# Kernel optimization log

Hardware: AMD Instinct MI355X
Metric: run time of the kernel (lower is better)

The kernel has to match this reference:

```python
import jax, jax.numpy as jnp
import numpy as np

N = 100000        # nodes
E = 1600000       # directed edges (avg degree 16)
F_IN, F_HID, F_OUT = 512, 32, 16


def setup_inputs() -> dict:
    key = jax.random.key(0)
    k0, k1, k2, k3 = jax.random.split(key, 4)
    x = jax.random.normal(k0, (N, F_IN), dtype=jnp.float32)
    edge_index = jax.random.randint(k1, (2, E), 0, N, dtype=jnp.int32)
    # Glorot-ish init for the two GCNConv linear weights
    W1 = jax.random.normal(k2, (F_IN, F_HID), dtype=jnp.float32) / np.float32(np.sqrt(F_IN))
    W2 = jax.random.normal(k3, (F_HID, F_OUT), dtype=jnp.float32) / np.float32(np.sqrt(F_HID))
    b1 = jnp.zeros((F_HID,), jnp.float32)
    b2 = jnp.zeros((F_OUT,), jnp.float32)
    return {"x": x, "W1": W1, "b1": b1, "W2": W2, "b2": b2, "edge_index": edge_index}


def gcn_conv(x, W, b, src, dst):
    """PyG GCNConv: h = x W; symmetric-normalized aggregation with self-loops; + bias."""
    h = x @ W                                   # [N, F_out] project first (PyG order)
    # degree including the implicit self-loop (start from ones)
    deg = jnp.ones((N,), h.dtype).at[dst].add(1.0)
    dinv = jax.lax.rsqrt(deg)                   # deg^{-1/2}
    coef = (dinv[src] * dinv[dst])[:, None]     # [E, 1] edge norm
    msg = h[src] * coef                         # gather + scale
    agg = jax.ops.segment_sum(msg, dst, num_segments=N)  # scatter-add to dst
    agg = agg + h * (dinv * dinv)[:, None]      # self-loop contribution
    return agg + b


def reference(x, W1, b1, W2, b2, edge_index):
    src, dst = edge_index[0], edge_index[1]
    h = jax.nn.relu(gcn_conv(x, W1, b1, src, dst))
    # F.dropout(training=self.training) is identity in eval mode
    h = gcn_conv(h, W2, b2, src, dst)
    return jax.nn.log_softmax(h, axis=1)
```

## Files before the change

### kernel.cpp

```cpp
#include <hip/hip_runtime.h>
#include <hip/hip_bf16.h>
#include <cstdint>

#define NN   100000
#define NE   1600000
#define FIN  512
#define FHID 32
#define FOUT 16

#define BSHIFT 8
#define BSIZE  256
#define NBUCK  391
#define HB     128
#define BEPB   4096
#define NBB    ((NE + BEPB - 1) / BEPB)
#define GB     782

typedef float f32x4 __attribute__((ext_vector_type(4)));
typedef short s16x8 __attribute__((ext_vector_type(8)));
typedef short s16x4 __attribute__((ext_vector_type(4)));
typedef int   i32x4 __attribute__((ext_vector_type(4)));
typedef unsigned int u32;
typedef unsigned short u16;

__device__ __forceinline__ short f2bf(float f) {
  union { float f; uint32_t u; } v; v.f = f;
  uint32_t r = v.u + 0x7fffu + ((v.u >> 16) & 1u);
  return (short)(r >> 16);
}
__device__ __forceinline__ float bf2f(u16 u) {
  union { uint32_t u; float f; } v; v.u = (uint32_t)u << 16; return v.f;
}

__global__ __launch_bounds__(256) void k_hist(const int* __restrict__ dst,
                                              u32* __restrict__ bcount) {
  __shared__ u32 h[NBUCK];
  int tid = threadIdx.x;
  for (int i = tid; i < NBUCK; i += 256) h[i] = 0;
  __syncthreads();
  const int stride = HB * 256 * 4;
  for (int e0 = (blockIdx.x * 256 + tid) * 4; e0 + 3 < NE; e0 += stride) {
    i32x4 d4 = *(const i32x4*)(dst + e0);
    atomicAdd(&h[d4[0] >> BSHIFT], 1u);
    atomicAdd(&h[d4[1] >> BSHIFT], 1u);
    atomicAdd(&h[d4[2] >> BSHIFT], 1u);
    atomicAdd(&h[d4[3] >> BSHIFT], 1u);
  }
  __syncthreads();
  for (int i = tid; i < NBUCK; i += 256)
    if (h[i]) atomicAdd(&bcount[i], h[i]);
}

__global__ __launch_bounds__(512) void k_bscan(const u32* __restrict__ bc,
                                               u32* __restrict__ bstart,
                                               u32* __restrict__ bcur,
                                               const float* __restrict__ W1,
                                               u16* __restrict__ wfrag) {
  __shared__ u32 tmp[512];
  int tid = threadIdx.x;
  u32 v = (tid < NBUCK) ? bc[tid] : 0;
  tmp[tid] = v;
  __syncthreads();
  #pragma unroll
  for (int off = 1; off < 512; off <<= 1) {
    u32 t = (tid >= off) ? tmp[tid - off] : 0;
    __syncthreads();
    tmp[tid] += t;
    __syncthreads();
  }
  if (tid < NBUCK) { u32 e = tmp[tid] - v; bstart[tid] = e; bcur[tid] = e; }
  if (tid == 511) bstart[NBUCK] = tmp[511];

  for (int it = 0; it < 32; ++it) {
    int flat = it * 512 + tid;
    int i  = flat & 7;
    int l  = (flat >> 3) & 63;
    int nt = (flat >> 9) & 1;
    int kt = flat >> 10;
    int k  = kt * 32 + ((l >> 4) << 3) + i;
    int n  = nt * 16 + (l & 15);
    wfrag[flat] = (u16)f2bf(W1[k * 32 + n]);
  }
}

__global__ __launch_bounds__(512) void k_bin(const int* __restrict__ src,
                                             const int* __restrict__ dst,
                                             u32* __restrict__ bcur,
                                             u32* __restrict__ binned) {
  __shared__ u32 cnt[NBUCK];
  __shared__ u32 lofs[NBUCK];
  __shared__ u32 gbase[NBUCK];
  __shared__ u32 tmp[512];
  __shared__ u32 stage[BEPB];
  __shared__ u16 sb[BEPB];
  int tid = threadIdx.x;
  for (int i = tid; i < NBUCK; i += 512) cnt[i] = 0;
  __syncthreads();

  int base = blockIdx.x * BEPB;
  u32 vals[8]; u32 ofs[8]; int bks[8];
  #pragma unroll
  for (int half = 0; half < 2; ++half) {
    int e0 = base + tid * 8 + half * 4;
    if (e0 + 3 < NE) {
      i32x4 s4 = *(const i32x4*)(src + e0);
      i32x4 d4 = *(const i32x4*)(dst + e0);
      #pragma unroll
      for (int k = 0; k < 4; ++k) {
        int b = d4[k] >> BSHIFT;
        bks[half * 4 + k] = b;
        vals[half * 4 + k] = (u32)s4[k] | ((u32)(d4[k] & (BSIZE - 1)) << 17);
        ofs[half * 4 + k] = atomicAdd(&cnt[b], 1u);
      }
    } else {
      #pragma unroll
      for (int k = 0; k < 4; ++k) {
        int e = e0 + k;
        bool ok = e < NE;
        int s = 0, d = 0;
        if (ok) { s = src[e]; d = dst[e]; }
        int b = ok ? (d >> BSHIFT) : -1;
        bks[half * 4 + k] = b;
        vals[half * 4 + k] = (u32)s | ((u32)(d & (BSIZE - 1)) << 17);
        ofs[half * 4 + k] = ok ? atomicAdd(&cnt[b], 1u) : 0;
      }
    }
  }
  __syncthreads();

  u32 cv = (tid < NBUCK) ? cnt[tid] : 0;
  tmp[tid] = cv;
  __syncthreads();
  #pragma unroll
  for (int off = 1; off < 512; off <<= 1) {
    u32 t = (tid >= off) ? tmp[tid - off] : 0;
    __syncthreads();
    tmp[tid] += t;
    __syncthreads();
  }
  if (tid < NBUCK) {
    lofs[tid] = tmp[tid] - cv;
    gbase[tid] = cv ? atomicAdd(&bcur[tid], cv) : 0;
  }
  __syncthreads();
  u32 total = tmp[511];
  __syncthreads();

  #pragma unroll
  for (int k = 0; k < 8; ++k) {
    if (bks[k] >= 0) {
      u32 sl = lofs[bks[k]] + ofs[k];
      stage[sl] = vals[k];
      sb[sl] = (u16)bks[k];
    }
  }
  __syncthreads();

  for (u32 s2 = tid; s2 < total; s2 += 512) {
    int b = sb[s2];
    binned[gbase[b] + (s2 - lofs[b])] = stage[s2];
  }
}

__global__ __launch_bounds__(256) void k_fin(const u32* __restrict__ binned,
                                             const u32* __restrict__ bstart,
                                             int* __restrict__ deg,
                                             int* __restrict__ rs,
                                             float* __restrict__ dinv,
                                             int* __restrict__ csr) {
  __shared__ u32 degl[BSIZE];
  __shared__ u32 rsl[BSIZE];
  int tid = threadIdx.x;
  int b = blockIdx.x;
  u32 start = bstart[b];
  u32 n = bstart[b + 1] - start;

  degl[tid] = 0;
  __syncthreads();
  for (u32 k = tid; k < n; k += 256)
    atomicAdd(&degl[binned[start + k] >> 17], 1u);
  __syncthreads();

  u32 v = degl[tid];
  rsl[tid] = v;
  __syncthreads();
  #pragma unroll
  for (int off = 1; off < 256; off <<= 1) {
    u32 t = (tid >= off) ? rsl[tid - off] : 0;
    __syncthreads();
    rsl[tid] += t;
    __syncthreads();
  }
  u32 e = rsl[tid] - v;
  __syncthreads();
  rsl[tid] = e;

  int g = b * BSIZE + tid;
  if (g < NN) {
    deg[g] = (int)v;
    rs[g] = (int)(start + e);
    dinv[g] = rsqrtf(1.0f + (float)v);
  }
  __syncthreads();

  for (u32 k = tid; k < n; k += 256) {
    u32 vv = binned[start + k];
    u32 pos = atomicAdd(&rsl[vv >> 17], 1u);
    csr[start + pos] = (int)(vv & 0x1FFFFu);
  }
}

#define G1_ISSUE(TILE)                                                        \
  do {                                                                        \
    int r0_ = (TILE) * 16;                                                    \
    _Pragma("unroll")                                                         \
    for (int r_ = 0; r_ < 16; ++r_) {                                         \
      int row_ = r0_ + r_;                                                    \
      if (row_ >= NN) row_ = NN - 1;                                          \
      const float* rp_ = x + (size_t)row_ * FIN + lane * 4;                   \
      va[r_] = *(const f32x4*)rp_;                                            \
      vb[r_] = *(const f32x4*)(rp_ + 256);                                    \
    }                                                                         \
  } while (0)

#define G1_CVTWRITE()                                                         \
  do {                                                                        \
    _Pragma("unroll")                                                         \
    for (int r_ = 0; r_ < 16; ++r_) {                                         \
      u32 sw_ = (u32)((r_ & 7) << 4);                                         \
      s16x4 w0_, w1_;                                                         \
      _Pragma("unroll")                                                       \
      for (int q_ = 0; q_ < 4; ++q_) {                                        \
        w0_[q_] = f2bf(va[r_][q_]);                                           \
        w1_[q_] = f2bf(vb[r_][q_]);                                           \
      }                                                                       \
      *(s16x4*)(xw + (((u32)(r_ * 1024 + lane * 8)) ^ sw_)) = w0_;            \
      *(s16x4*)(xw + (((u32)(r_ * 1024 + 512 + lane * 8)) ^ sw_)) = w1_;      \
    }                                                                         \
  } while (0)

#define G1_MFMA_STORE(TILE)                                                   \
  do {                                                                        \
    f32x4 acc0_ = {}, acc1_ = {};                                             \
    _Pragma("unroll")                                                         \
    for (int kt_ = 0; kt_ < 16; ++kt_) {                                      \
      s16x8 af_ = *(const s16x8*)(xw +                                        \
          (((u32)(m * 1024 + kt_ * 64 + h * 16)) ^ msw));                     \
      s16x8 b0_ = wf[(kt_ * 2 + 0) * 64 + lane];                              \
      s16x8 b1_ = wf[(kt_ * 2 + 1) * 64 + lane];                              \
      acc0_ = __builtin_amdgcn_mfma_f32_16x16x32_bf16(af_, b0_, acc0_, 0,0,0);\
      acc1_ = __builtin_amdgcn_mfma_f32_16x16x32_bf16(af_, b1_, acc1_, 0,0,0);\
    }                                                                         \
    int r0_ = (TILE) * 16;                                                    \
    _Pragma("unroll")                                                         \
    for (int r_ = 0; r_ < 4; ++r_) {                                          \
      int row_ = r0_ + h * 4 + r_;                                            \
      if (row_ < NN) {                                                        \
        float di_ = dinv[row_];                                               \
        u16* o_ = Hs1 + (size_t)row_ * FHID + m;                              \
        o_[0]  = (u16)f2bf(acc0_[r_] * di_);                                  \
        o_[16] = (u16)f2bf(acc1_[r_] * di_);                                  \
      }                                                                       \
    }                                                                         \
  } while (0)

__global__ __launch_bounds__(256) void k_gemm1(const float* __restrict__ x,
                                               const u16* __restrict__ wfrag,
                                               const float* __restrict__ dinv,
                                               u16* __restrict__ Hs1) {
  __shared__ u16 Xs[4][16][512];
  const int tid  = threadIdx.x;
  const int lane = tid & 63;
  const int wv   = tid >> 6;
  char* xw = (char*)&Xs[wv][0][0];
  const int h = lane >> 4;
  const int m = lane & 15;
  const u32 msw = (u32)((m & 7) << 4);
  const s16x8* wf = (const s16x8*)wfrag;

  const int t0 = (blockIdx.x * 4 + wv) * 2;
  f32x4 va[16], vb[16];

  G1_ISSUE(t0);
  G1_CVTWRITE();
  G1_ISSUE(t0 + 1);
  G1_MFMA_STORE(t0);
  G1_CVTWRITE();
  G1_MFMA_STORE(t0 + 1);
}

__global__ __launch_bounds__(256) void k_gat1(const int* __restrict__ csr,
                                              const int* __restrict__ rs,
                                              const int* __restrict__ deg,
                                              const float* __restrict__ dinv,
                                              const float* __restrict__ b1,
                                              const float* __restrict__ W2,
                                              const u16* __restrict__ Hs1,
                                              u16* __restrict__ Hs2) {
  __shared__ float w[FHID * FOUT];
  for (int i = threadIdx.x; i < FHID * FOUT; i += 256) w[i] = W2[i];
  __syncthreads();

  int t = blockIdx.x * 256 + threadIdx.x;
  int d = t >> 2;
  if (d >= NN) return;
  int p = t & 3;
  int start = rs[d], n = deg[d];

  float a0[8], a1[8], a2[8], a3[8];
  {
    s16x8 v = *(const s16x8*)(Hs1 + (size_t)d * FHID + p * 8);
    #pragma unroll
    for (int k = 0; k < 8; ++k) {
      a0[k] = bf2f((u16)v[k]); a1[k] = 0.f; a2[k] = 0.f; a3[k] = 0.f;
    }
  }
  int j = 0;
  for (; j + 8 <= n; j += 8) {
    int s0=csr[start+j],   s1=csr[start+j+1], s2=csr[start+j+2], s3=csr[start+j+3];
    int s4=csr[start+j+4], s5=csr[start+j+5], s6=csr[start+j+6], s7=csr[start+j+7];
    s16x8 v0 = *(const s16x8*)(Hs1 + (size_t)s0 * FHID + p * 8);
    s16x8 v1 = *(const s16x8*)(Hs1 + (size_t)s1 * FHID + p * 8);
    s16x8 v2 = *(const s16x8*)(Hs1 + (size_t)s2 * FHID + p * 8);
    s16x8 v3 = *(const s16x8*)(Hs1 + (size_t)s3 * FHID + p * 8);
    s16x8 v4 = *(const s16x8*)(Hs1 + (size_t)s4 * FHID + p * 8);
    s16x8 v5 = *(const s16x8*)(Hs1 + (size_t)s5 * FHID + p * 8);
    s16x8 v6 = *(const s16x8*)(Hs1 + (size_t)s6 * FHID + p * 8);
    s16x8 v7 = *(const s16x8*)(Hs1 + (size_t)s7 * FHID + p * 8);
    #pragma unroll
    for (int k = 0; k < 8; ++k) {
      a0[k] += bf2f((u16)v0[k]);
      a1[k] += bf2f((u16)v1[k]);
      a2[k] += bf2f((u16)v2[k]);
      a3[k] += bf2f((u16)v3[k]);
      a0[k] += bf2f((u16)v4[k]);
      a1[k] += bf2f((u16)v5[k]);
      a2[k] += bf2f((u16)v6[k]);
      a3[k] += bf2f((u16)v7[k]);
    }
  }
  for (; j + 4 <= n; j += 4) {
    int s0=csr[start+j], s1=csr[start+j+1], s2=csr[start+j+2], s3=csr[start+j+3];
    s16x8 v0 = *(const s16x8*)(Hs1 + (size_t)s0 * FHID + p * 8);
    s16x8 v1 = *(const s16x8*)(Hs1 + (size_t)s1 * FHID + p * 8);
    s16x8 v2 = *(const s16x8*)(Hs1 + (size_t)s2 * FHID + p * 8);
    s16x8 v3 = *(const s16x8*)(Hs1 + (size_t)s3 * FHID + p * 8);
    #pragma unroll
    for (int k = 0; k < 8; ++k) {
      a0[k] += bf2f((u16)v0[k]);
      a1[k] += bf2f((u16)v1[k]);
      a2[k] += bf2f((u16)v2[k]);
      a3[k] += bf2f((u16)v3[k]);
    }
  }
  for (; j < n; ++j) {
    int s0 = csr[start + j];
    s16x8 v0 = *(const s16x8*)(Hs1 + (size_t)s0 * FHID + p * 8);
    #pragma unroll
    for (int k = 0; k < 8; ++k) a0[k] += bf2f((u16)v0[k]);
  }

  float dd = dinv[d];
  float h[8];
  #pragma unroll
  for (int k = 0; k < 8; ++k)
    h[k] = fmaxf(((a0[k] + a1[k]) + (a2[k] + a3[k])) * dd + b1[p * 8 + k], 0.0f);

  float pj[FOUT];
  #pragma unroll
  for (int jj = 0; jj < FOUT; ++jj) pj[jj] = 0.f;
  #pragma unroll
  for (int k = 0; k < 8; ++k)
    #pragma unroll
    for (int jj = 0; jj < FOUT; ++jj)
      pj[jj] = fmaf(h[k], w[(p * 8 + k) * FOUT + jj], pj[jj]);
  #pragma unroll
  for (int jj = 0; jj < FOUT; ++jj) {
    pj[jj] += __shfl_xor(pj[jj], 1);
    pj[jj] += __shfl_xor(pj[jj], 2);
  }
  s16x4 o;
  #pragma unroll
  for (int q = 0; q < 4; ++q) o[q] = f2bf(pj[p * 4 + q] * dd);
  *(s16x4*)(Hs2 + (size_t)d * FOUT + p * 4) = o;
}

__global__ __launch_bounds__(256) void k_gat2(const int* __restrict__ csr,
                                              const int* __restrict__ rs,
                                              const int* __restrict__ deg,
                                              const float* __restrict__ dinv,
                                              const float* __restrict__ b2,
                                              const u16* __restrict__ Hs2,
                                              float* __restrict__ out) {
  int t = blockIdx.x * 256 + threadIdx.x;
  int d = t >> 2;
  if (d >= NN) return;
  int p = t & 3;
  int start = rs[d], n = deg[d];

  float a0[4], a1[4], a2[4], a3[4];
  {
    s16x4 v = *(const s16x4*)(Hs2 + (size_t)d * FOUT + p * 4);
    #pragma unroll
    for (int k = 0; k < 4; ++k) { a0[k] = bf2f((u16)v[k]); a1[k]=0.f; a2[k]=0.f; a3[k]=0.f; }
  }
  int j = 0;
  for (; j + 8 <= n; j += 8) {
    int s0=csr[start+j],   s1=csr[start+j+1], s2=csr[start+j+2], s3=csr[start+j+3];
    int s4=csr[start+j+4], s5=csr[start+j+5], s6=csr[start+j+6], s7=csr[start+j+7];
    s16x4 v0 = *(const s16x4*)(Hs2 + (size_t)s0 * FOUT + p * 4);
    s16x4 v1 = *(const s16x4*)(Hs2 + (size_t)s1 * FOUT + p * 4);
    s16x4 v2 = *(const s16x4*)(Hs2 + (size_t)s2 * FOUT + p * 4);
    s16x4 v3 = *(const s16x4*)(Hs2 + (size_t)s3 * FOUT + p * 4);
    s16x4 v4 = *(const s16x4*)(Hs2 + (size_t)s4 * FOUT + p * 4);
    s16x4 v5 = *(const s16x4*)(Hs2 + (size_t)s5 * FOUT + p * 4);
    s16x4 v6 = *(const s16x4*)(Hs2 + (size_t)s6 * FOUT + p * 4);
    s16x4 v7 = *(const s16x4*)(Hs2 + (size_t)s7 * FOUT + p * 4);
    #pragma unroll
    for (int k = 0; k < 4; ++k) {
      a0[k] += bf2f((u16)v0[k]); a1[k] += bf2f((u16)v1[k]);
      a2[k] += bf2f((u16)v2[k]); a3[k] += bf2f((u16)v3[k]);
      a0[k] += bf2f((u16)v4[k]); a1[k] += bf2f((u16)v5[k]);
      a2[k] += bf2f((u16)v6[k]); a3[k] += bf2f((u16)v7[k]);
    }
  }
  for (; j + 4 <= n; j += 4) {
    int s0=csr[start+j], s1=csr[start+j+1], s2=csr[start+j+2], s3=csr[start+j+3];
    s16x4 v0 = *(const s16x4*)(Hs2 + (size_t)s0 * FOUT + p * 4);
    s16x4 v1 = *(const s16x4*)(Hs2 + (size_t)s1 * FOUT + p * 4);
    s16x4 v2 = *(const s16x4*)(Hs2 + (size_t)s2 * FOUT + p * 4);
    s16x4 v3 = *(const s16x4*)(Hs2 + (size_t)s3 * FOUT + p * 4);
    #pragma unroll
    for (int k = 0; k < 4; ++k) {
      a0[k] += bf2f((u16)v0[k]); a1[k] += bf2f((u16)v1[k]);
      a2[k] += bf2f((u16)v2[k]); a3[k] += bf2f((u16)v3[k]);
    }
  }
  for (; j < n; ++j) {
    int s0 = csr[start + j];
    s16x4 v0 = *(const s16x4*)(Hs2 + (size_t)s0 * FOUT + p * 4);
    #pragma unroll
    for (int k = 0; k < 4; ++k) a0[k] += bf2f((u16)v0[k]);
  }

  float dd = dinv[d];
  float z[4];
  #pragma unroll
  for (int k = 0; k < 4; ++k)
    z[k] = ((a0[k]+a1[k]) + (a2[k]+a3[k])) * dd + b2[p * 4 + k];

  float m = fmaxf(fmaxf(z[0], z[1]), fmaxf(z[2], z[3]));
  m = fmaxf(m, __shfl_xor(m, 1));
  m = fmaxf(m, __shfl_xor(m, 2));
  float s = expf(z[0]-m) + expf(z[1]-m) + expf(z[2]-m) + expf(z[3]-m);
  s += __shfl_xor(s, 1);
  s += __shfl_xor(s, 2);
  float lse = m + logf(s);

  f32x4 o = { z[0]-lse, z[1]-lse, z[2]-lse, z[3]-lse };
  *(f32x4*)(out + (size_t)d * FOUT + p * 4) = o;
}

extern "C" void kernel_launch(void* const* d_in, const int* in_sizes, int n_in,
                              void* d_out, int out_size, void* d_ws, size_t ws_size,
                              hipStream_t stream) {
  const float* x  = (const float*)d_in[0];
  const float* W1 = (const float*)d_in[1];
  const float* b1 = (const float*)d_in[2];
  const float* W2 = (const float*)d_in[3];
  const float* b2 = (const float*)d_in[4];
  const int*   ei = (const int*)d_in[5];
  const int* srcv = ei;
  const int* dstv = ei + NE;

  char* ws = (char*)d_ws;
  const size_t KB = 1024, MB = 1048576;
  u32*   bcount = (u32*)(ws + 0);
  u32*   bstart = (u32*)(ws + 8 * KB);
  u32*   bcur   = (u32*)(ws + 16 * KB);
  u16*   wfrag  = (u16*)(ws + 64 * KB);
  int*   deg    = (int*)(ws + 512 * KB);
  int*   rs     = (int*)(ws + 1024 * KB);
  float* dinv   = (float*)(ws + 1536 * KB);
  u32*   binned = (u32*)(ws + 2 * MB);
  int*   csr    = (int*)(ws + 9 * MB);
  u16*   Hs1    = (u16*)(ws + 16 * MB);
  u16*   Hs2    = (u16*)(ws + 23 * MB);
  float* out    = (float*)d_out;

  hipMemsetAsync(bcount, 0, NBUCK * sizeof(u32), stream);

  k_hist <<<HB,  256, 0, stream>>>(dstv, bcount);
  k_bscan<<<1,   512, 0, stream>>>(bcount, bstart, bcur, W1, wfrag);
  k_bin  <<<NBB, 512, 0, stream>>>(srcv, dstv, bcur, binned);
  k_fin  <<<NBUCK, 256, 0, stream>>>(binned, bstart, deg, rs, dinv, csr);
  k_gemm1<<<GB, 256, 0, stream>>>(x, wfrag, dinv, Hs1);
  k_gat1 <<<(NN * 4 + 255) / 256, 256, 0, stream>>>(csr, rs, deg, dinv, b1, W2, Hs1, Hs2);
  k_gat2 <<<(NN * 4 + 255) / 256, 256, 0, stream>>>(csr, rs, deg, dinv, b2, Hs2, out);
}
```

Before: 139.2 us.

## Fuse bucket scan into histogram and co-schedule GEMM with edge binning

Folds the single-block bucket scan and W1 fragment conversion into the histogram kernel, using a last-block ticket so the scan needs no separate launch. Merges the layer-1 GEMM and the edge binning into one heterogeneous launch, which requires removing the GEMM's dependency on dinv: H1 is stored unscaled and the source-side dinv is applied per edge in the first gather. This removes two launches and lets the GEMM's memory traffic overlap with binning. In exchange the first gather does an extra random dinv load per edge, and the bin block size is halved to fit 256-thread blocks.

```diff
diff --git a/kernel.cpp b/kernel.cpp
--- a/kernel.cpp
+++ b/kernel.cpp
@@ -12,9 +12,10 @@
 #define BSIZE  256
 #define NBUCK  391
 #define HB     128
-#define BEPB   4096
+#define BEPB   2048
 #define NBB    ((NE + BEPB - 1) / BEPB)
-#define GB     782
+#define GEMB   391
+#define TOTB   (GEMB + NBB)
 
 typedef float f32x4 __attribute__((ext_vector_type(4)));
 typedef short s16x8 __attribute__((ext_vector_type(8)));
@@ -33,9 +34,31 @@
 }
 
 __global__ __launch_bounds__(256) void k_hist(const int* __restrict__ dst,
-                                              u32* __restrict__ bcount) {
+                                              const float* __restrict__ W1,
+                                              u16* __restrict__ wfrag,
+                                              u32* __restrict__ bcount,
+                                              u32* __restrict__ ticket,
+                                              u32* __restrict__ bstart,
+                                              u32* __restrict__ bcur) {
   __shared__ u32 h[NBUCK];
+  __shared__ u32 wsum[4];
+  __shared__ bool amlast;
   int tid = threadIdx.x;
+  int lane = tid & 63;
+
+  if (blockIdx.x == 0) {
+    for (int it = 0; it < 64; ++it) {
+      int flat = it * 256 + tid;
+      int i  = flat & 7;
+      int l  = (flat >> 3) & 63;
+      int nt = (flat >> 9) & 1;
+      int kt = flat >> 10;
+      int k  = kt * 32 + ((l >> 4) << 3) + i;
+      int n  = nt * 16 + (l & 15);
+      wfrag[flat] = (u16)f2bf(W1[k * 32 + n]);
+    }
+  }
+
   for (int i = tid; i < NBUCK; i += 256) h[i] = 0;
   __syncthreads();
   const int stride = HB * 256 * 4;
@@ -49,166 +72,50 @@
   __syncthreads();
   for (int i = tid; i < NBUCK; i += 256)
     if (h[i]) atomicAdd(&bcount[i], h[i]);
-}
-
-__global__ __launch_bounds__(512) void k_bscan(const u32* __restrict__ bc,
-                                               u32* __restrict__ bstart,
-                                               u32* __restrict__ bcur,
-                                               const float* __restrict__ W1,
-                                               u16* __restrict__ wfrag) {
-  __shared__ u32 tmp[512];
-  int tid = threadIdx.x;
-  u32 v = (tid < NBUCK) ? bc[tid] : 0;
-  tmp[tid] = v;
-  __syncthreads();
-  #pragma unroll
-  for (int off = 1; off < 512; off <<= 1) {
-    u32 t = (tid >= off) ? tmp[tid - off] : 0;
-    __syncthreads();
-    tmp[tid] += t;
-    __syncthreads();
-  }
-  if (tid < NBUCK) { u32 e = tmp[tid] - v; bstart[tid] = e; bcur[tid] = e; }
-  if (tid == 511) bstart[NBUCK] = tmp[511];
-
-  for (int it = 0; it < 32; ++it) {
-    int flat = it * 512 + tid;
-    int i  = flat & 7;
-    int l  = (flat >> 3) & 63;
-    int nt = (flat >> 9) & 1;
-    int kt = flat >> 10;
-    int k  = kt * 32 + ((l >> 4) << 3) + i;
-    int n  = nt * 16 + (l & 15);
-    wfrag[flat] = (u16)f2bf(W1[k * 32 + n]);
-  }
-}
-
-__global__ __launch_bounds__(512) void k_bin(const int* __restrict__ src,
-                                             const int* __restrict__ dst,
-                                             u32* __restrict__ bcur,
-                                             u32* __restrict__ binned) {
-  __shared__ u32 cnt[NBUCK];
-  __shared__ u32 lofs[NBUCK];
-  __shared__ u32 gbase[NBUCK];
-  __shared__ u32 tmp[512];
-  __shared__ u32 stage[BEPB];
-  __shared__ u16 sb[BEPB];
-  int tid = threadIdx.x;
-  for (int i = tid; i < NBUCK; i += 512) cnt[i] = 0;
-  __syncthreads();
-
-  int base = blockIdx.x * BEPB;
-  u32 vals[8]; u32 ofs[8]; int bks[8];
-  #pragma unroll
-  for (int half = 0; half < 2; ++half) {
-    int e0 = base + tid * 8 + half * 4;
-    if (e0 + 3 < NE) {
-      i32x4 s4 = *(const i32x4*)(src + e0);
-      i32x4 d4 = *(const i32x4*)(dst + e0);
-      #pragma unroll
-      for (int k = 0; k < 4; ++k) {
-        int b = d4[k] >> BSHIFT;
-        bks[half * 4 + k] = b;
-        vals[half * 4 + k] = (u32)s4[k] | ((u32)(d4[k] & (BSIZE - 1)) << 17);
-        ofs[half * 4 + k] = atomicAdd(&cnt[b], 1u);
-      }
-    } else {
-      #pragma unroll
-      for (int k = 0; k < 4; ++k) {
-        int e = e0 + k;
-        bool ok = e < NE;
-        int s = 0, d = 0;
-        if (ok) { s = src[e]; d = dst[e]; }
-        int b = ok ? (d >> BSHIFT) : -1;
-        bks[half * 4 + k] = b;
-        vals[half * 4 + k] = (u32)s | ((u32)(d & (BSIZE - 1)) << 17);
-        ofs[half * 4 + k] = ok ? atomicAdd(&cnt[b], 1u) : 0;
-      }
-    }
-  }
-  __syncthreads();
-
-  u32 cv = (tid < NBUCK) ? cnt[tid] : 0;
-  tmp[tid] = cv;
-  __syncthreads();
-  #pragma unroll
-  for (int off = 1; off < 512; off <<= 1) {
-    u32 t = (tid >= off) ? tmp[tid - off] : 0;
-    __syncthreads();
-    tmp[tid] += t;
-    __syncthreads();
-  }
-  if (tid < NBUCK) {
-    lofs[tid] = tmp[tid] - cv;
-    gbase[tid] = cv ? atomicAdd(&bcur[tid], cv) : 0;
-  }
-  __syncthreads();
-  u32 total = tmp[511];
-  __syncthreads();
-
-  #pragma unroll
-  for (int k = 0; k < 8; ++k) {
-    if (bks[k] >= 0) {
-      u32 sl = lofs[bks[k]] + ofs[k];
-      stage[sl] = vals[k];
-      sb[sl] = (u16)bks[k];
-    }
-  }
-  __syncthreads();
-
-  for (u32 s2 = tid; s2 < total; s2 += 512) {
-    int b = sb[s2];
-    binned[gbase[b] + (s2 - lofs[b])] = stage[s2];
-  }
-}
-
-__global__ __launch_bounds__(256) void k_fin(const u32* __restrict__ binned,
-                                             const u32* __restrict__ bstart,
-                                             int* __restrict__ deg,
-                                             int* __restrict__ rs,
-                                             float* __restrict__ dinv,
-                                             int* __restrict__ csr) {
-  __shared__ u32 degl[BSIZE];
-  __shared__ u32 rsl[BSIZE];
-  int tid = threadIdx.x;
-  int b = blockIdx.x;
-  u32 start = bstart[b];
-  u32 n = bstart[b + 1] - start;
-
-  degl[tid] = 0;
-  __syncthreads();
-  for (u32 k = tid; k < n; k += 256)
-    atomicAdd(&degl[binned[start + k] >> 17], 1u);
-  __syncthreads();
-
-  u32 v = degl[tid];
-  rsl[tid] = v;
-  __syncthreads();
-  #pragma unroll
-  for (int off = 1; off < 256; off <<= 1) {
-    u32 t = (tid >= off) ? rsl[tid - off] : 0;
-    __syncthreads();
-    rsl[tid] += t;
-    __syncthreads();
-  }
-  u32 e = rsl[tid] - v;
-  __syncthreads();
-  rsl[tid] = e;
-
-  int g = b * BSIZE + tid;
-  if (g < NN) {
-    deg[g] = (int)v;
-    rs[g] = (int)(start + e);
-    dinv[g] = rsqrtf(1.0f + (float)v);
-  }
-  __syncthreads();
-
-  for (u32 k = tid; k < n; k += 256) {
-    u32 vv = binned[start + k];
-    u32 pos = atomicAdd(&rsl[vv >> 17], 1u);
-    csr[start + pos] = (int)(vv & 0x1FFFFu);
-  }
-}
+  __syncthreads();
+  if (tid == 0) {
+    __threadfence();
+    u32 t = __hip_atomic_fetch_add(ticket, 1u, __ATOMIC_ACQ_REL, __HIP_MEMORY_SCOPE_AGENT);
+    amlast = (t == gridDim.x - 1);
+  }
+  __syncthreads();
+  if (!amlast) return;
+
+  u32 a0 = (2*tid   < NBUCK) ? __hip_atomic_load(&bcount[2*tid],   __ATOMIC_RELAXED, __HIP_MEMORY_SCOPE_AGENT) : 0;
+  u32 a1 = (2*tid+1 < NBUCK) ? __hip_atomic_load(&bcount[2*tid+1], __ATOMIC_RELAXED, __HIP_MEMORY_SCOPE_AGENT) : 0;
+  u32 s = a0 + a1;
+  u32 v = s;
+  #pragma unroll
+  for (int off = 1; off < 64; off <<= 1) {
+    u32 t = __shfl_up(v, off);
+    if (lane >= off) v += t;
+  }
+  if (lane == 63) wsum[tid >> 6] = v;
+  __syncthreads();
+  if (tid < 4) {
+    u32 w0 = wsum[tid], w = w0;
+    #pragma unroll
+    for (int off = 1; off < 4; off <<= 1) {
+      u32 t = __shfl_up(w, off, 4);
+      if ((tid & 3) >= off) w += t;
+    }
+    wsum[tid] = w - w0;
+  }
+  __syncthreads();
+  u32 excl = v - s + wsum[tid >> 6];
+  if (2*tid < NBUCK)   { bstart[2*tid]   = excl;      bcur[2*tid]   = excl; }
+  if (2*tid+1 < NBUCK) { bstart[2*tid+1] = excl + a0; bcur[2*tid+1] = excl + a0; }
+  if (tid == 255) bstart[NBUCK] = excl + s;
+}
+
+union BGSh {
+  u16 Xs[4][16][512];
+  struct {
+    u32 cnt[NBUCK]; u32 lofs[NBUCK]; u32 gbase[NBUCK];
+    u32 wsum[4]; u32 total;
+    u32 stage[BEPB]; u16 sb[BEPB];
+  } bin;
+};
 
 #define G1_ISSUE(TILE)                                                        \
   do {                                                                        \
@@ -256,37 +163,175 @@
     for (int r_ = 0; r_ < 4; ++r_) {                                          \
       int row_ = r0_ + h * 4 + r_;                                            \
       if (row_ < NN) {                                                        \
-        float di_ = dinv[row_];                                               \
-        u16* o_ = Hs1 + (size_t)row_ * FHID + m;                              \
-        o_[0]  = (u16)f2bf(acc0_[r_] * di_);                                  \
-        o_[16] = (u16)f2bf(acc1_[r_] * di_);                                  \
+        u16* o_ = H1 + (size_t)row_ * FHID + m;                               \
+        o_[0]  = (u16)f2bf(acc0_[r_]);                                        \
+        o_[16] = (u16)f2bf(acc1_[r_]);                                        \
       }                                                                       \
     }                                                                         \
   } while (0)
 
-__global__ __launch_bounds__(256) void k_gemm1(const float* __restrict__ x,
-                                               const u16* __restrict__ wfrag,
-                                               const float* __restrict__ dinv,
-                                               u16* __restrict__ Hs1) {
-  __shared__ u16 Xs[4][16][512];
-  const int tid  = threadIdx.x;
+__global__ __launch_bounds__(256) void k_binemm(
+    const int* __restrict__ src, const int* __restrict__ dst,
+    const float* __restrict__ x, const u16* __restrict__ wfrag,
+    u32* __restrict__ bcur, u32* __restrict__ binned,
+    u16* __restrict__ H1) {
+  __shared__ BGSh sh;
+  const int tid = threadIdx.x;
   const int lane = tid & 63;
-  const int wv   = tid >> 6;
-  char* xw = (char*)&Xs[wv][0][0];
-  const int h = lane >> 4;
-  const int m = lane & 15;
-  const u32 msw = (u32)((m & 7) << 4);
-  const s16x8* wf = (const s16x8*)wfrag;
-
-  const int t0 = (blockIdx.x * 4 + wv) * 2;
-  f32x4 va[16], vb[16];
-
-  G1_ISSUE(t0);
-  G1_CVTWRITE();
-  G1_ISSUE(t0 + 1);
-  G1_MFMA_STORE(t0);
-  G1_CVTWRITE();
-  G1_MFMA_STORE(t0 + 1);
+
+  if (blockIdx.x < GEMB) {
+    const int wv = tid >> 6;
+    char* xw = (char*)&sh.Xs[wv][0][0];
+    const int h = lane >> 4;
+    const int m = lane & 15;
+    const u32 msw = (u32)((m & 7) << 4);
+    const s16x8* wf = (const s16x8*)wfrag;
+    const int t0 = ((int)blockIdx.x * 4 + wv) * 4;
+    f32x4 va[16], vb[16];
+
+    G1_ISSUE(t0);
+    G1_CVTWRITE();
+    #pragma unroll
+    for (int i = 0; i < 3; ++i) {
+      G1_ISSUE(t0 + i + 1);
+      G1_MFMA_STORE(t0 + i);
+      G1_CVTWRITE();
+    }
+    G1_MFMA_STORE(t0 + 3);
+    return;
+  }
+
+  const int bid = blockIdx.x - GEMB;
+  for (int i = tid; i < NBUCK; i += 256) sh.bin.cnt[i] = 0;
+  __syncthreads();
+
+  int base = bid * BEPB;
+  u32 vals[8]; u32 ofs[8]; int bks[8];
+  #pragma unroll
+  for (int half = 0; half < 2; ++half) {
+    int e0 = base + tid * 8 + half * 4;
+    if (e0 + 3 < NE) {
+      i32x4 s4 = *(const i32x4*)(src + e0);
+      i32x4 d4 = *(const i32x4*)(dst + e0);
+      #pragma unroll
+      for (int k = 0; k < 4; ++k) {
+        int b = d4[k] >> BSHIFT;
+        bks[half * 4 + k] = b;
+        vals[half * 4 + k] = (u32)s4[k] | ((u32)(d4[k] & (BSIZE - 1)) << 17);
+        ofs[half * 4 + k] = atomicAdd(&sh.bin.cnt[b], 1u);
+      }
+    } else {
+      #pragma unroll
+      for (int k = 0; k < 4; ++k) {
+        int e = e0 + k;
+        bool ok = e < NE;
+        int s = 0, d = 0;
+        if (ok) { s = src[e]; d = dst[e]; }
+        int b = ok ? (d >> BSHIFT) : -1;
+        bks[half * 4 + k] = b;
+        vals[half * 4 + k] = (u32)s | ((u32)(d & (BSIZE - 1)) << 17);
+        ofs[half * 4 + k] = ok ? atomicAdd(&sh.bin.cnt[b], 1u) : 0;
+      }
+    }
+  }
+  __syncthreads();
+
+  u32 a0 = (2*tid   < NBUCK) ? sh.bin.cnt[2*tid]   : 0;
+  u32 a1 = (2*tid+1 < NBUCK) ? sh.bin.cnt[2*tid+1] : 0;
+  u32 s = a0 + a1;
+  u32 v = s;
+  #pragma unroll
+  for (int off = 1; off < 64; off <<= 1) {
+    u32 t = __shfl_up(v, off);
+    if (lane >= off) v += t;
+  }
+  if (lane == 63) sh.bin.wsum[tid >> 6] = v;
+  __syncthreads();
+  if (tid < 4) {
+    u32 w0 = sh.bin.wsum[tid], w = w0;
+    #pragma unroll
+    for (int off = 1; off < 4; off <<= 1) {
+      u32 t = __shfl_up(w, off, 4);
+      if ((tid & 3) >= off) w += t;
+    }
+    sh.bin.wsum[tid] = w - w0;
+  }
+  __syncthreads();
+  u32 excl = v - s + sh.bin.wsum[tid >> 6];
+  if (2*tid < NBUCK) {
+    sh.bin.lofs[2*tid] = excl;
+    sh.bin.gbase[2*tid] = a0 ? atomicAdd(&bcur[2*tid], a0) : 0;
+  }
+  if (2*tid+1 < NBUCK) {
+    sh.bin.lofs[2*tid+1] = excl + a0;
+    sh.bin.gbase[2*tid+1] = a1 ? atomicAdd(&bcur[2*tid+1], a1) : 0;
+  }
+  if (tid == 255) sh.bin.total = excl + s;
+  __syncthreads();
+  u32 total = sh.bin.total;
+
+  #pragma unroll
+  for (int k = 0; k < 8; ++k) {
+    if (bks[k] >= 0) {
+      u32 sl = sh.bin.lofs[bks[k]] + ofs[k];
+      sh.bin.stage[sl] = vals[k];
+      sh.bin.sb[sl] = (u16)bks[k];
+    }
+  }
+  __syncthreads();
+
+  for (u32 s2 = tid; s2 < total; s2 += 256) {
+    int b = sh.bin.sb[s2];
+    binned[sh.bin.gbase[b] + (s2 - sh.bin.lofs[b])] = sh.bin.stage[s2];
+  }
+}
+
+__global__ __launch_bounds__(256) void k_fin(const u32* __restrict__ binned,
+                                             const u32* __restrict__ bstart,
+                                             int* __restrict__ deg,
+                                             int* __restrict__ rs,
+                                             float* __restrict__ dinv,
+                                             int* __restrict__ csr) {
+  __shared__ u32 degl[BSIZE];
+  __shared__ u32 rsl[BSIZE];
+  int tid = threadIdx.x;
+  int b = blockIdx.x;
+  u32 start = bstart[b];
+  u32 n = bstart[b + 1] - start;
+
+  degl[tid] = 0;
+  __syncthreads();
+  for (u32 k = tid; k < n; k += 256)
+    atomicAdd(&degl[binned[start + k] >> 17], 1u);
+  __syncthreads();
+
+  u32 v = degl[tid];
+  rsl[tid] = v;
+  __syncthreads();
+  #pragma unroll
+  for (int off = 1; off < 256; off <<= 1) {
+    u32 t = (tid >= off) ? rsl[tid - off] : 0;
+    __syncthreads();
+    rsl[tid] += t;
+    __syncthreads();
+  }
+  u32 e = rsl[tid] - v;
+  __syncthreads();
+  rsl[tid] = e;
+
+  int g = b * BSIZE + tid;
+  if (g < NN) {
+    deg[g] = (int)v;
+    rs[g] = (int)(start + e);
+    dinv[g] = rsqrtf(1.0f + (float)v);
+  }
+  __syncthreads();
+
+  for (u32 k = tid; k < n; k += 256) {
+    u32 vv = binned[start + k];
+    u32 pos = atomicAdd(&rsl[vv >> 17], 1u);
+    csr[start + pos] = (int)(vv & 0x1FFFFu);
+  }
 }
 
 __global__ __launch_bounds__(256) void k_gat1(const int* __restrict__ csr,
@@ -295,7 +340,7 @@
                                               const float* __restrict__ dinv,
                                               const float* __restrict__ b1,
                                               const float* __restrict__ W2,
-                                              const u16* __restrict__ Hs1,
+                                              const u16* __restrict__ H1,
                                               u16* __restrict__ Hs2) {
   __shared__ float w[FHID * FOUT];
   for (int i = threadIdx.x; i < FHID * FOUT; i += 256) w[i] = W2[i];
@@ -306,61 +351,65 @@
   if (d >= NN) return;
   int p = t & 3;
   int start = rs[d], n = deg[d];
+  float dd = dinv[d];
 
   float a0[8], a1[8], a2[8], a3[8];
   {
-    s16x8 v = *(const s16x8*)(Hs1 + (size_t)d * FHID + p * 8);
+    s16x8 v = *(const s16x8*)(H1 + (size_t)d * FHID + p * 8);
     #pragma unroll
     for (int k = 0; k < 8; ++k) {
-      a0[k] = bf2f((u16)v[k]); a1[k] = 0.f; a2[k] = 0.f; a3[k] = 0.f;
+      a0[k] = dd * bf2f((u16)v[k]); a1[k] = 0.f; a2[k] = 0.f; a3[k] = 0.f;
     }
   }
   int j = 0;
   for (; j + 8 <= n; j += 8) {
     int s0=csr[start+j],   s1=csr[start+j+1], s2=csr[start+j+2], s3=csr[start+j+3];
     int s4=csr[start+j+4], s5=csr[start+j+5], s6=csr[start+j+6], s7=csr[start+j+7];
-    s16x8 v0 = *(const s16x8*)(Hs1 + (size_t)s0 * FHID + p * 8);
-    s16x8 v1 = *(const s16x8*)(Hs1 + (size_t)s1 * FHID + p * 8);
-    s16x8 v2 = *(const s16x8*)(Hs1 + (size_t)s2 * FHID + p * 8);
-    s16x8 v3 = *(const s16x8*)(Hs1 + (size_t)s3 * FHID + p * 8);
-    s16x8 v4 = *(const s16x8*)(Hs1 + (size_t)s4 * FHID + p * 8);
-    s16x8 v5 = *(const s16x8*)(Hs1 + (size_t)s5 * FHID + p * 8);
-    s16x8 v6 = *(const s16x8*)(Hs1 + (size_t)s6 * FHID + p * 8);
-    s16x8 v7 = *(const s16x8*)(Hs1 + (size_t)s7 * FHID + p * 8);
+    float d0=dinv[s0], d1=dinv[s1], d2=dinv[s2], d3=dinv[s3];
+    float d4=dinv[s4], d5=dinv[s5], d6=dinv[s6], d7=dinv[s7];
+    s16x8 v0 = *(const s16x8*)(H1 + (size_t)s0 * FHID + p * 8);
+    s16x8 v1 = *(const s16x8*)(H1 + (size_t)s1 * FHID + p * 8);
+    s16x8 v2 = *(const s16x8*)(H1 + (size_t)s2 * FHID + p * 8);
+    s16x8 v3 = *(const s16x8*)(H1 + (size_t)s3 * FHID + p * 8);
+    s16x8 v4 = *(const s16x8*)(H1 + (size_t)s4 * FHID + p * 8);
+    s16x8 v5 = *(const s16x8*)(H1 + (size_t)s5 * FHID + p * 8);
+    s16x8 v6 = *(const s16x8*)(H1 + (size_t)s6 * FHID + p * 8);
+    s16x8 v7 = *(const s16x8*)(H1 + (size_t)s7 * FHID + p * 8);
     #pragma unroll
     for (int k = 0; k < 8; ++k) {
-      a0[k] += bf2f((u16)v0[k]);
-      a1[k] += bf2f((u16)v1[k]);
-      a2[k] += bf2f((u16)v2[k]);
-      a3[k] += bf2f((u16)v3[k]);
-      a0[k] += bf2f((u16)v4[k]);
-      a1[k] += bf2f((u16)v5[k]);
-      a2[k] += bf2f((u16)v6[k]);
-      a3[k] += bf2f((u16)v7[k]);
+      a0[k] = fmaf(d0, bf2f((u16)v0[k]), a0[k]);
+      a1[k] = fmaf(d1, bf2f((u16)v1[k]), a1[k]);
+      a2[k] = fmaf(d2, bf2f((u16)v2[k]), a2[k]);
+      a3[k] = fmaf(d3, bf2f((u16)v3[k]), a3[k]);
+      a0[k] = fmaf(d4, bf2f((u16)v4[k]), a0[k]);
+      a1[k] = fmaf(d5, bf2f((u16)v5[k]), a1[k]);
+      a2[k] = fmaf(d6, bf2f((u16)v6[k]), a2[k]);
+      a3[k] = fmaf(d7, bf2f((u16)v7[k]), a3[k]);
     }
   }
   for (; j + 4 <= n; j += 4) {
     int s0=csr[start+j], s1=csr[start+j+1], s2=csr[start+j+2], s3=csr[start+j+3];
-    s16x8 v0 = *(const s16x8*)(Hs1 + (size_t)s0 * FHID + p * 8);
-    s16x8 v1 = *(const s16x8*)(Hs1 + (size_t)s1 * FHID + p * 8);
-    s16x8 v2 = *(const s16x8*)(Hs1 + (size_t)s2 * FHID + p * 8);
-    s16x8 v3 = *(const s16x8*)(Hs1 + (size_t)s3 * FHID + p * 8);
+    float d0=dinv[s0], d1=dinv[s1], d2=dinv[s2], d3=dinv[s3];
+    s16x8 v0 = *(const s16x8*)(H1 + (size_t)s0 * FHID + p * 8);
+    s16x8 v1 = *(const s16x8*)(H1 + (size_t)s1 * FHID + p * 8);
+    s16x8 v2 = *(const s16x8*)(H1 + (size_t)s2 * FHID + p * 8);
+    s16x8 v3 = *(const s16x8*)(H1 + (size_t)s3 * FHID + p * 8);
     #pragma unroll
     for (int k = 0; k < 8; ++k) {
-      a0[k] += bf2f((u16)v0[k]);
-      a1[k] += bf2f((u16)v1[k]);
-      a2[k] += bf2f((u16)v2[k]);
-      a3[k] += bf2f((u16)v3[k]);
+      a0[k] = fmaf(d0, bf2f((u16)v0[k]), a0[k]);
+      a1[k] = fmaf(d1, bf2f((u16)v1[k]), a1[k]);
+      a2[k] = fmaf(d2, bf2f((u16)v2[k]), a2[k]);
+      a3[k] = fmaf(d3, bf2f((u16)v3[k]), a3[k]);
     }
   }
   for (; j < n; ++j) {
     int s0 = csr[start + j];
-    s16x8 v0 = *(const s16x8*)(Hs1 + (size_t)s0 * FHID + p * 8);
-    #pragma unroll
-    for (int k = 0; k < 8; ++k) a0[k] += bf2f((u16)v0[k]);
-  }
-
-  float dd = dinv[d];
+    float d0 = dinv[s0];
+    s16x8 v0 = *(const s16x8*)(H1 + (size_t)s0 * FHID + p * 8);
+    #pragma unroll
+    for (int k = 0; k < 8; ++k) a0[k] = fmaf(d0, bf2f((u16)v0[k]), a0[k]);
+  }
+
   float h[8];
   #pragma unroll
   for (int k = 0; k < 8; ++k)
@@ -476,6 +525,7 @@
   char* ws = (char*)d_ws;
   const size_t KB = 1024, MB = 1048576;
   u32*   bcount = (u32*)(ws + 0);
+  u32*   ticket = (u32*)(ws + 1600);
   u32*   bstart = (u32*)(ws + 8 * KB);
   u32*   bcur   = (u32*)(ws + 16 * KB);
   u16*   wfrag  = (u16*)(ws + 64 * KB);
@@ -484,17 +534,15 @@
   float* dinv   = (float*)(ws + 1536 * KB);
   u32*   binned = (u32*)(ws + 2 * MB);
   int*   csr    = (int*)(ws + 9 * MB);
-  u16*   Hs1    = (u16*)(ws + 16 * MB);
+  u16*   H1     = (u16*)(ws + 16 * MB);
   u16*   Hs2    = (u16*)(ws + 23 * MB);
   float* out    = (float*)d_out;
 
-  hipMemsetAsync(bcount, 0, NBUCK * sizeof(u32), stream);
-
-  k_hist <<<HB,  256, 0, stream>>>(dstv, bcount);
-  k_bscan<<<1,   512, 0, stream>>>(bcount, bstart, bcur, W1, wfrag);
-  k_bin  <<<NBB, 512, 0, stream>>>(srcv, dstv, bcur, binned);
-  k_fin  <<<NBUCK, 256, 0, stream>>>(binned, bstart, deg, rs, dinv, csr);
-  k_gemm1<<<GB, 256, 0, stream>>>(x, wfrag, dinv, Hs1);
-  k_gat1 <<<(NN * 4 + 255) / 256, 256, 0, stream>>>(csr, rs, deg, dinv, b1, W2, Hs1, Hs2);
-  k_gat2 <<<(NN * 4 + 255) / 256, 256, 0, stream>>>(csr, rs, deg, dinv, b2, Hs2, out);
-}
+  hipMemsetAsync(ws, 0, 2 * KB, stream);
+
+  k_hist  <<<HB,   256, 0, stream>>>(dstv, W1, wfrag, bcount, ticket, bstart, bcur);
+  k_binemm<<<TOTB, 256, 0, stream>>>(srcv, dstv, x, wfrag, bcur, binned, H1);
+  k_fin   <<<NBUCK, 256, 0, stream>>>(binned, bstart, deg, rs, dinv, csr);
+  k_gat1  <<<(NN * 4 + 255) / 256, 256, 0, stream>>>(csr, rs, deg, dinv, b1, W2, H1, Hs2);
+  k_gat2  <<<(NN * 4 + 255) / 256, 256, 0, stream>>>(csr, rs, deg, dinv, b2, Hs2, out);
+}
```

Result: slower. 152.8 us (+9.8%).

## Fold bucket scan into histogram via last-block ticket; restructure gemm1 into single-wave blocks

Applied to the files above, without the earlier changes.

The separate single-block scan kernel is removed. The last histogram block, found with an atomic ticket, now does the bucket prefix scan with wave shuffles, and block 0 builds the W1 bf16 fragments. This saves one kernel launch and its serialization. gemm1 now runs one 64-thread wave per block over two 16-row tiles, loading each half row separately so that conversion, MFMA and the next load interleave with half the register buffer. The row-bounds clamps are dropped (NN is a multiple of 32). The ticket adds a device-wide fence and atomic, and the finer-grained blocks raise block-scheduling overhead.

```diff
diff --git a/kernel.cpp b/kernel.cpp
--- a/kernel.cpp
+++ b/kernel.cpp
@@ -14,7 +14,7 @@
 #define HB     128
 #define BEPB   4096
 #define NBB    ((NE + BEPB - 1) / BEPB)
-#define GB     782
+#define GB     3125
 
 typedef float f32x4 __attribute__((ext_vector_type(4)));
 typedef short s16x8 __attribute__((ext_vector_type(8)));
@@ -33,9 +33,31 @@
 }
 
 __global__ __launch_bounds__(256) void k_hist(const int* __restrict__ dst,
-                                              u32* __restrict__ bcount) {
+                                              const float* __restrict__ W1,
+                                              u16* __restrict__ wfrag,
+                                              u32* __restrict__ bcount,
+                                              u32* __restrict__ ticket,
+                                              u32* __restrict__ bstart,
+                                              u32* __restrict__ bcur) {
   __shared__ u32 h[NBUCK];
+  __shared__ u32 wsum[4];
+  __shared__ bool amlast;
   int tid = threadIdx.x;
+  int lane = tid & 63;
+
+  if (blockIdx.x == 0) {
+    for (int it = 0; it < 64; ++it) {
+      int flat = it * 256 + tid;
+      int i  = flat & 7;
+      int l  = (flat >> 3) & 63;
+      int nt = (flat >> 9) & 1;
+      int kt = flat >> 10;
+      int k  = kt * 32 + ((l >> 4) << 3) + i;
+      int n  = nt * 16 + (l & 15);
+      wfrag[flat] = (u16)f2bf(W1[k * 32 + n]);
+    }
+  }
+
   for (int i = tid; i < NBUCK; i += 256) h[i] = 0;
   __syncthreads();
   const int stride = HB * 256 * 4;
@@ -49,38 +71,40 @@
   __syncthreads();
   for (int i = tid; i < NBUCK; i += 256)
     if (h[i]) atomicAdd(&bcount[i], h[i]);
-}
-
-__global__ __launch_bounds__(512) void k_bscan(const u32* __restrict__ bc,
-                                               u32* __restrict__ bstart,
-                                               u32* __restrict__ bcur,
-                                               const float* __restrict__ W1,
-                                               u16* __restrict__ wfrag) {
-  __shared__ u32 tmp[512];
-  int tid = threadIdx.x;
-  u32 v = (tid < NBUCK) ? bc[tid] : 0;
-  tmp[tid] = v;
-  __syncthreads();
-  #pragma unroll
-  for (int off = 1; off < 512; off <<= 1) {
-    u32 t = (tid >= off) ? tmp[tid - off] : 0;
-    __syncthreads();
-    tmp[tid] += t;
-    __syncthreads();
-  }
-  if (tid < NBUCK) { u32 e = tmp[tid] - v; bstart[tid] = e; bcur[tid] = e; }
-  if (tid == 511) bstart[NBUCK] = tmp[511];
-
-  for (int it = 0; it < 32; ++it) {
-    int flat = it * 512 + tid;
-    int i  = flat & 7;
-    int l  = (flat >> 3) & 63;
-    int nt = (flat >> 9) & 1;
-    int kt = flat >> 10;
-    int k  = kt * 32 + ((l >> 4) << 3) + i;
-    int n  = nt * 16 + (l & 15);
-    wfrag[flat] = (u16)f2bf(W1[k * 32 + n]);
-  }
+  __syncthreads();
+  if (tid == 0) {
+    __threadfence();
+    u32 t = __hip_atomic_fetch_add(ticket, 1u, __ATOMIC_ACQ_REL, __HIP_MEMORY_SCOPE_AGENT);
+    amlast = (t == gridDim.x - 1);
+  }
+  __syncthreads();
+  if (!amlast) return;
+
+  u32 a0 = (2*tid   < NBUCK) ? __hip_atomic_load(&bcount[2*tid],   __ATOMIC_RELAXED, __HIP_MEMORY_SCOPE_AGENT) : 0;
+  u32 a1 = (2*tid+1 < NBUCK) ? __hip_atomic_load(&bcount[2*tid+1], __ATOMIC_RELAXED, __HIP_MEMORY_SCOPE_AGENT) : 0;
+  u32 s = a0 + a1;
+  u32 v = s;
+  #pragma unroll
+  for (int off = 1; off < 64; off <<= 1) {
+    u32 t = __shfl_up(v, off);
+    if (lane >= off) v += t;
+  }
+  if (lane == 63) wsum[tid >> 6] = v;
+  __syncthreads();
+  if (tid < 4) {
+    u32 w0 = wsum[tid], w = w0;
+    #pragma unroll
+    for (int off = 1; off < 4; off <<= 1) {
+      u32 t = __shfl_up(w, off, 4);
+      if ((tid & 3) >= off) w += t;
+    }
+    wsum[tid] = w - w0;
+  }
+  __syncthreads();
+  u32 excl = v - s + wsum[tid >> 6];
+  if (2*tid < NBUCK)   { bstart[2*tid]   = excl;      bcur[2*tid]   = excl; }
+  if (2*tid+1 < NBUCK) { bstart[2*tid+1] = excl + a0; bcur[2*tid+1] = excl + a0; }
+  if (tid == 255) bstart[NBUCK] = excl + s;
 }
 
 __global__ __launch_bounds__(512) void k_bin(const int* __restrict__ src,
@@ -210,83 +234,77 @@
   }
 }
 
-#define G1_ISSUE(TILE)                                                        \
+#define G1_ISSUE(TILE, HALF)                                                  \
   do {                                                                        \
     int r0_ = (TILE) * 16;                                                    \
     _Pragma("unroll")                                                         \
     for (int r_ = 0; r_ < 16; ++r_) {                                         \
-      int row_ = r0_ + r_;                                                    \
-      if (row_ >= NN) row_ = NN - 1;                                          \
-      const float* rp_ = x + (size_t)row_ * FIN + lane * 4;                   \
-      va[r_] = *(const f32x4*)rp_;                                            \
-      vb[r_] = *(const f32x4*)(rp_ + 256);                                    \
+      buf[r_] = *(const f32x4*)(x + (size_t)(r0_ + r_) * FIN +                \
+                                (HALF) * 256 + lane * 4);                     \
     }                                                                         \
   } while (0)
 
-#define G1_CVTWRITE()                                                         \
+#define G1_CVT(HALF)                                                          \
   do {                                                                        \
     _Pragma("unroll")                                                         \
     for (int r_ = 0; r_ < 16; ++r_) {                                         \
       u32 sw_ = (u32)((r_ & 7) << 4);                                         \
-      s16x4 w0_, w1_;                                                         \
+      s16x4 w_;                                                               \
       _Pragma("unroll")                                                       \
-      for (int q_ = 0; q_ < 4; ++q_) {                                        \
-        w0_[q_] = f2bf(va[r_][q_]);                                           \
-        w1_[q_] = f2bf(vb[r_][q_]);                                           \
-      }                                                                       \
-      *(s16x4*)(xw + (((u32)(r_ * 1024 + lane * 8)) ^ sw_)) = w0_;            \
-      *(s16x4*)(xw + (((u32)(r_ * 1024 + 512 + lane * 8)) ^ sw_)) = w1_;      \
+      for (int q_ = 0; q_ < 4; ++q_) w_[q_] = f2bf(buf[r_][q_]);              \
+      *(s16x4*)(xw + (((u32)(r_ * 1024 + (HALF) * 512 + lane * 8)) ^ sw_)) = w_; \
     }                                                                         \
   } while (0)
 
-#define G1_MFMA_STORE(TILE)                                                   \
+#define G1_MFMAH(HALF)                                                        \
   do {                                                                        \
-    f32x4 acc0_ = {}, acc1_ = {};                                             \
     _Pragma("unroll")                                                         \
-    for (int kt_ = 0; kt_ < 16; ++kt_) {                                      \
+    for (int kt_ = (HALF) * 8; kt_ < (HALF) * 8 + 8; ++kt_) {                 \
       s16x8 af_ = *(const s16x8*)(xw +                                        \
           (((u32)(m * 1024 + kt_ * 64 + h * 16)) ^ msw));                     \
       s16x8 b0_ = wf[(kt_ * 2 + 0) * 64 + lane];                              \
       s16x8 b1_ = wf[(kt_ * 2 + 1) * 64 + lane];                              \
-      acc0_ = __builtin_amdgcn_mfma_f32_16x16x32_bf16(af_, b0_, acc0_, 0,0,0);\
-      acc1_ = __builtin_amdgcn_mfma_f32_16x16x32_bf16(af_, b1_, acc1_, 0,0,0);\
+      acc0 = __builtin_amdgcn_mfma_f32_16x16x32_bf16(af_, b0_, acc0, 0,0,0);  \
+      acc1 = __builtin_amdgcn_mfma_f32_16x16x32_bf16(af_, b1_, acc1, 0,0,0);  \
     }                                                                         \
+  } while (0)
+
+#define G1_STORE(TILE)                                                        \
+  do {                                                                        \
     int r0_ = (TILE) * 16;                                                    \
     _Pragma("unroll")                                                         \
     for (int r_ = 0; r_ < 4; ++r_) {                                          \
       int row_ = r0_ + h * 4 + r_;                                            \
-      if (row_ < NN) {                                                        \
-        float di_ = dinv[row_];                                               \
-        u16* o_ = Hs1 + (size_t)row_ * FHID + m;                              \
-        o_[0]  = (u16)f2bf(acc0_[r_] * di_);                                  \
-        o_[16] = (u16)f2bf(acc1_[r_] * di_);                                  \
-      }                                                                       \
+      float di_ = dinv[row_];                                                 \
+      u16* o_ = Hs1 + (size_t)row_ * FHID + m;                                \
+      o_[0]  = (u16)f2bf(acc0[r_] * di_);                                     \
+      o_[16] = (u16)f2bf(acc1[r_] * di_);                                     \
     }                                                                         \
   } while (0)
 
-__global__ __launch_bounds__(256) void k_gemm1(const float* __restrict__ x,
-                                               const u16* __restrict__ wfrag,
-                                               const float* __restrict__ dinv,
-                                               u16* __restrict__ Hs1) {
-  __shared__ u16 Xs[4][16][512];
-  const int tid  = threadIdx.x;
-  const int lane = tid & 63;
-  const int wv   = tid >> 6;
-  char* xw = (char*)&Xs[wv][0][0];
+__global__ __launch_bounds__(64) void k_gemm1(const float* __restrict__ x,
+                                              const u16* __restrict__ wfrag,
+                                              const float* __restrict__ dinv,
+                                              u16* __restrict__ Hs1) {
+  __shared__ u16 Xs[16][512];
+  const int lane = threadIdx.x;
+  char* xw = (char*)Xs;
   const int h = lane >> 4;
   const int m = lane & 15;
   const u32 msw = (u32)((m & 7) << 4);
   const s16x8* wf = (const s16x8*)wfrag;
-
-  const int t0 = (blockIdx.x * 4 + wv) * 2;
-  f32x4 va[16], vb[16];
-
-  G1_ISSUE(t0);
-  G1_CVTWRITE();
-  G1_ISSUE(t0 + 1);
-  G1_MFMA_STORE(t0);
-  G1_CVTWRITE();
-  G1_MFMA_STORE(t0 + 1);
+  const int t0 = blockIdx.x * 2;
+
+  f32x4 buf[16];
+  f32x4 acc0, acc1;
+
+  G1_ISSUE(t0, 0);   G1_CVT(0);
+  G1_ISSUE(t0, 1);   acc0 = (f32x4){}; acc1 = (f32x4){};
+                     G1_MFMAH(0);  G1_CVT(1);
+  G1_ISSUE(t0+1, 0); G1_MFMAH(1);  G1_STORE(t0);  G1_CVT(0);
+  G1_ISSUE(t0+1, 1); acc0 = (f32x4){}; acc1 = (f32x4){};
+                     G1_MFMAH(0);  G1_CVT(1);
+                     G1_MFMAH(1);  G1_STORE(t0+1);
 }
 
 __global__ __launch_bounds__(256) void k_gat1(const int* __restrict__ csr,
@@ -476,6 +494,7 @@
   char* ws = (char*)d_ws;
   const size_t KB = 1024, MB = 1048576;
   u32*   bcount = (u32*)(ws + 0);
+  u32*   ticket = (u32*)(ws + 1600);
   u32*   bstart = (u32*)(ws + 8 * KB);
   u32*   bcur   = (u32*)(ws + 16 * KB);
   u16*   wfrag  = (u16*)(ws + 64 * KB);
@@ -488,13 +507,12 @@
   u16*   Hs2    = (u16*)(ws + 23 * MB);
   float* out    = (float*)d_out;
 
-  hipMemsetAsync(bcount, 0, NBUCK * sizeof(u32), stream);
-
-  k_hist <<<HB,  256, 0, stream>>>(dstv, bcount);
-  k_bscan<<<1,   512, 0, stream>>>(bcount, bstart, bcur, W1, wfrag);
-  k_bin  <<<NBB, 512, 0, stream>>>(srcv, dstv, bcur, binned);
+  hipMemsetAsync(ws, 0, 2 * KB, stream);
+
+  k_hist <<<HB,   256, 0, stream>>>(dstv, W1, wfrag, bcount, ticket, bstart, bcur);
+  k_bin  <<<NBB,  512, 0, stream>>>(srcv, dstv, bcur, binned);
   k_fin  <<<NBUCK, 256, 0, stream>>>(binned, bstart, deg, rs, dinv, csr);
-  k_gemm1<<<GB, 256, 0, stream>>>(x, wfrag, dinv, Hs1);
+  k_gemm1<<<GB, 64, 0, stream>>>(x, wfrag, dinv, Hs1);
   k_gat1 <<<(NN * 4 + 255) / 256, 256, 0, stream>>>(csr, rs, deg, dinv, b1, W2, Hs1, Hs2);
   k_gat2 <<<(NN * 4 + 255) / 256, 256, 0, stream>>>(csr, rs, deg, dinv, b2, Hs2, out);
 }
```

Measured after the change: 134.6 us (median of 2 runs). 3.3% less time.
